# Performance work log

Hardware: AMD Instinct MI355X
Metric: run time of the kernel (lower is better)

## Reference

```python
import jax, jax.numpy as jnp
import numpy as np

D_IN = 256
DIMS = 256


def setup_inputs() -> dict:
    key = jax.random.key(0)
    k1, k2, k3, k4, k5 = jax.random.split(key, 5)
    B, Tq, Tk = 4, 512, 512
    query = jax.random.normal(k1, (B, Tq, D_IN), dtype=jnp.float32)
    value = jax.random.normal(k2, (B, Tk, D_IN), dtype=jnp.float32)
    # Dense(dims, use_bias=False) kernels (glorot-like scale) and AdditiveAttention scale vector
    Wq = jax.random.normal(k3, (D_IN, DIMS), dtype=jnp.float32) / np.sqrt(D_IN)
    Wv = jax.random.normal(k4, (D_IN, DIMS), dtype=jnp.float32) / np.sqrt(D_IN)
    scale = jax.random.normal(k5, (DIMS,), dtype=jnp.float32)
    return {"query": query, "value": value, "Wq": Wq, "Wv": Wv, "scale": scale}


def reference(query, value, Wq, Wv, scale):
    # q_proj: [B,Tq,d], k_proj: [B,Tk,d]; attention value = RAW value tensor (as in source)
    q = jnp.einsum("bqi,id->bqd", query, Wq)
    k = jnp.einsum("bki,id->bkd", value, Wv)
    # Additive (Bahdanau) scores: [B,Tq,Tk] via broadcast tanh then reduce with scale
    scores = jnp.einsum("bqkd,d->bqk", jnp.tanh(q[:, :, None, :] + k[:, None, :, :]), scale)
    attn = jax.nn.softmax(scores, axis=-1)  # masks are all-ones -> no-op
    out = jnp.einsum("bqk,bki->bqi", attn, value)
    return out, attn
```

## Files before the change

### kernel.cpp

```cpp
#include <hip/hip_runtime.h>

#define LOG2E 1.4426950408889634f
#define TWO_LOG2E 2.885390081777927f

__device__ __forceinline__ float fast_exp2(float x) { return __builtin_amdgcn_exp2f(x); }
__device__ __forceinline__ float fast_rcp(float x)  { return __builtin_amdgcn_rcpf(x); }

__global__ __launch_bounds__(256) void proj_kernel(
    const float* __restrict__ query, const float* __restrict__ value,
    const float* __restrict__ Wq, const float* __restrict__ Wv,
    float* __restrict__ eq, float* __restrict__ ek)
{
    __shared__ float in_lds[8 * 256];
    const int t = threadIdx.x;
    const int row0 = blockIdx.x * 8;
    const float* src; const float* W; float* dst;
    if (row0 < 2048) { src = query + (size_t)row0 * 256; W = Wq; dst = eq + (size_t)row0 * 256; }
    else { const int r = row0 - 2048; src = value + (size_t)r * 256; W = Wv; dst = ek + (size_t)r * 256; }

    const float4* s4 = (const float4*)src;
    float4* l4 = (float4*)in_lds;
    l4[t] = s4[t];
    l4[t + 256] = s4[t + 256];
    __syncthreads();

    float acc[8];
#pragma unroll
    for (int r = 0; r < 8; ++r) acc[r] = 0.f;

    for (int d = 0; d < 256; d += 4) {
        const float w0 = W[(d + 0) * 256 + t];
        const float w1 = W[(d + 1) * 256 + t];
        const float w2 = W[(d + 2) * 256 + t];
        const float w3 = W[(d + 3) * 256 + t];
#pragma unroll
        for (int r = 0; r < 8; ++r) {
            const float4 v = *(const float4*)&in_lds[r * 256 + d];
            acc[r] = fmaf(v.x, w0, acc[r]);
            acc[r] = fmaf(v.y, w1, acc[r]);
            acc[r] = fmaf(v.z, w2, acc[r]);
            acc[r] = fmaf(v.w, w3, acc[r]);
        }
    }
#pragma unroll
    for (int r = 0; r < 8; ++r) dst[r * 256 + t] = fast_exp2(acc[r] * TWO_LOG2E);
}

#define SQ_ST 130
__global__ __launch_bounds__(512) void scores_kernel(
    const float* __restrict__ eq, const float* __restrict__ ek,
    const float* __restrict__ scale, float* __restrict__ sraw)
{
    __shared__ float q_lds[32 * SQ_ST];
    __shared__ float k_lds[64 * SQ_ST];
    __shared__ float sc_lds[256];

    const int t = threadIdx.x;
    const int tx = t & 31, ty = t >> 5;
    const int ktg = blockIdx.x, qt = blockIdx.y, b = blockIdx.z;
    const float* qbase = eq + (size_t)(b * 512 + qt * 32) * 256;
    const float* kbase = ek + (size_t)(b * 512 + ktg * 64) * 256;

    if (t < 256) sc_lds[t] = -2.f * scale[t];

    float a00 = 0.f, a01 = 0.f, a10 = 0.f, a11 = 0.f;

    for (int dc = 0; dc < 256; dc += 128) {
        __syncthreads();
#pragma unroll
        for (int l = 0; l < 2; ++l) {
            const int idx = t + 512 * l;
            const int row = idx >> 5, c4 = (idx & 31) * 4;
            const float4 v = *(const float4*)&qbase[row * 256 + dc + c4];
            *(float2*)&q_lds[row * SQ_ST + c4]     = make_float2(v.x, v.y);
            *(float2*)&q_lds[row * SQ_ST + c4 + 2] = make_float2(v.z, v.w);
        }
#pragma unroll
        for (int l = 0; l < 4; ++l) {
            const int idx = t + 512 * l;
            const int row = idx >> 5, c4 = (idx & 31) * 4;
            const float4 v = *(const float4*)&kbase[row * 256 + dc + c4];
            *(float2*)&k_lds[row * SQ_ST + c4]     = make_float2(v.x, v.y);
            *(float2*)&k_lds[row * SQ_ST + c4 + 2] = make_float2(v.z, v.w);
        }
        __syncthreads();

#pragma unroll 4
        for (int d = 0; d < 128; d += 2) {
            const float2 s2 = *(const float2*)&sc_lds[dc + d];
            const float2 qa = *(const float2*)&q_lds[(ty * 2 + 0) * SQ_ST + d];
            const float2 qb = *(const float2*)&q_lds[(ty * 2 + 1) * SQ_ST + d];
            const float2 ka = *(const float2*)&k_lds[tx * SQ_ST + d];
            const float2 kb = *(const float2*)&k_lds[(tx + 32) * SQ_ST + d];

            {
                const float A = fmaf(qa.x, ka.x, 1.f), B = fmaf(qa.y, ka.y, 1.f);
                a00 = fmaf(fmaf(s2.y, A, s2.x * B), fast_rcp(A * B), a00);
            }
            {
                const float A = fmaf(qa.x, kb.x, 1.f), B = fmaf(qa.y, kb.y, 1.f);
                a01 = fmaf(fmaf(s2.y, A, s2.x * B), fast_rcp(A * B), a01);
            }
            {
                const float A = fmaf(qb.x, ka.x, 1.f), B = fmaf(qb.y, ka.y, 1.f);
                a10 = fmaf(fmaf(s2.y, A, s2.x * B), fast_rcp(A * B), a10);
            }
            {
                const float A = fmaf(qb.x, kb.x, 1.f), B = fmaf(qb.y, kb.y, 1.f);
                a11 = fmaf(fmaf(s2.y, A, s2.x * B), fast_rcp(A * B), a11);
            }
        }
    }

    const int qrow = b * 512 + qt * 32 + ty * 2;
    const int kcol = ktg * 64 + tx;
    sraw[(size_t)(qrow + 0) * 512 + kcol]      = a00;
    sraw[(size_t)(qrow + 0) * 512 + kcol + 32] = a01;
    sraw[(size_t)(qrow + 1) * 512 + kcol]      = a10;
    sraw[(size_t)(qrow + 1) * 512 + kcol + 32] = a11;
}

#define SS_ROW 516
__global__ __launch_bounds__(512) void softpv_kernel(
    float* __restrict__ attn, const float* __restrict__ value,
    float* __restrict__ out)
{
    __shared__ float s_lds[8 * SS_ROW];
    __shared__ float red[4 * 8 * 256];
    __shared__ float inv_lds[8];

    const int t = threadIdx.x;
    const int w = t >> 6, lane = t & 63;
    const int qt = blockIdx.x, b = blockIdx.y;
    const int q0 = qt * 8;
    float* srow = attn + (size_t)(b * 512 + q0 + w) * 512;

    float e[8];
    float m = -1e30f;
#pragma unroll
    for (int j = 0; j < 8; ++j) {
        e[j] = srow[lane + 64 * j];
        m = fmaxf(m, e[j]);
    }
#pragma unroll
    for (int off = 32; off; off >>= 1) m = fmaxf(m, __shfl_xor(m, off));

    float sum = 0.f;
#pragma unroll
    for (int j = 0; j < 8; ++j) {
        e[j] = fast_exp2((e[j] - m) * LOG2E);
        sum += e[j];
    }
#pragma unroll
    for (int off = 32; off; off >>= 1) sum += __shfl_xor(sum, off);

    const float inv = fast_rcp(sum);
#pragma unroll
    for (int j = 0; j < 8; ++j) {
        s_lds[w * SS_ROW + lane + 64 * j] = e[j];
        srow[lane + 64 * j] = e[j] * inv;
    }
    if (lane == 0) inv_lds[w] = inv;
    __syncthreads();

    float4 acc[8];
#pragma unroll
    for (int r = 0; r < 8; ++r) acc[r] = make_float4(0.f, 0.f, 0.f, 0.f);

    const float* vbase = value + (size_t)(b * 512 + 64 * w) * 256;
    for (int k4 = 0; k4 < 64; k4 += 4) {
        const float4 v0 = *(const float4*)&vbase[(k4 + 0) * 256 + lane * 4];
        const float4 v1 = *(const float4*)&vbase[(k4 + 1) * 256 + lane * 4];
        const float4 v2 = *(const float4*)&vbase[(k4 + 2) * 256 + lane * 4];
        const float4 v3 = *(const float4*)&vbase[(k4 + 3) * 256 + lane * 4];
#pragma unroll
        for (int r = 0; r < 8; ++r) {
            const float4 s4 = *(const float4*)&s_lds[r * SS_ROW + 64 * w + k4];
            acc[r].x = fmaf(s4.x, v0.x, acc[r].x); acc[r].y = fmaf(s4.x, v0.y, acc[r].y);
            acc[r].z = fmaf(s4.x, v0.z, acc[r].z); acc[r].w = fmaf(s4.x, v0.w, acc[r].w);
            acc[r].x = fmaf(s4.y, v1.x, acc[r].x); acc[r].y = fmaf(s4.y, v1.y, acc[r].y);
            acc[r].z = fmaf(s4.y, v1.z, acc[r].z); acc[r].w = fmaf(s4.y, v1.w, acc[r].w);
            acc[r].x = fmaf(s4.z, v2.x, acc[r].x); acc[r].y = fmaf(s4.z, v2.y, acc[r].y);
            acc[r].z = fmaf(s4.z, v2.z, acc[r].z); acc[r].w = fmaf(s4.z, v2.w, acc[r].w);
            acc[r].x = fmaf(s4.w, v3.x, acc[r].x); acc[r].y = fmaf(s4.w, v3.y, acc[r].y);
            acc[r].z = fmaf(s4.w, v3.z, acc[r].z); acc[r].w = fmaf(s4.w, v3.w, acc[r].w);
        }
    }

    if (w >= 4) {
#pragma unroll
        for (int r = 0; r < 8; ++r)
            *(float4*)&red[((w - 4) * 8 + r) * 256 + lane * 4] = acc[r];
    }
    __syncthreads();
    if (w < 4) {
#pragma unroll
        for (int r = 0; r < 8; ++r) {
            const float4 o = *(const float4*)&red[(w * 8 + r) * 256 + lane * 4];
            acc[r].x += o.x; acc[r].y += o.y; acc[r].z += o.z; acc[r].w += o.w;
        }
    }
    __syncthreads();
    if (w >= 2 && w < 4) {
#pragma unroll
        for (int r = 0; r < 8; ++r)
            *(float4*)&red[((w - 2) * 8 + r) * 256 + lane * 4] = acc[r];
    }
    __syncthreads();
    if (w < 2) {
#pragma unroll
        for (int r = 0; r < 8; ++r) {
            const float4 o = *(const float4*)&red[(w * 8 + r) * 256 + lane * 4];
            acc[r].x += o.x; acc[r].y += o.y; acc[r].z += o.z; acc[r].w += o.w;
        }
    }
    __syncthreads();
    if (w == 1) {
#pragma unroll
        for (int r = 0; r < 8; ++r)
            *(float4*)&red[r * 256 + lane * 4] = acc[r];
    }
    __syncthreads();
    if (w == 0) {
#pragma unroll
        for (int r = 0; r < 8; ++r) {
            const float4 o = *(const float4*)&red[r * 256 + lane * 4];
            const float iv = inv_lds[r];
            float4 res;
            res.x = (acc[r].x + o.x) * iv;
            res.y = (acc[r].y + o.y) * iv;
            res.z = (acc[r].z + o.z) * iv;
            res.w = (acc[r].w + o.w) * iv;
            *(float4*)&out[(size_t)(b * 512 + q0 + r) * 256 + lane * 4] = res;
        }
    }
}

extern "C" void kernel_launch(void* const* d_in, const int* in_sizes, int n_in,
                              void* d_out, int out_size, void* d_ws, size_t ws_size,
                              hipStream_t stream) {
    const float* query = (const float*)d_in[0];
    const float* value = (const float*)d_in[1];
    const float* Wq    = (const float*)d_in[2];
    const float* Wv    = (const float*)d_in[3];
    const float* scale = (const float*)d_in[4];

    float* out0 = (float*)d_out;
    float* attn = out0 + 4 * 512 * 256;

    float* eq = (float*)d_ws;
    float* ek = eq + 2048 * 256;

    proj_kernel<<<512, 256, 0, stream>>>(query, value, Wq, Wv, eq, ek);
    scores_kernel<<<dim3(8, 16, 4), 512, 0, stream>>>(eq, ek, scale, attn);
    softpv_kernel<<<dim3(64, 4), 512, 0, stream>>>(attn, value, out0);
}
```

Baseline: 69.76 us.

## Fuse additive-score computation with softmax and PV into one kernel

Merges the separate scores kernel into the softmax/PV kernel. Each block now computes the full score rows for its 8 queries by streaming all 512 keys of its batch through LDS in 64-row tiles, then runs softmax and the PV product. This removes the raw-score round trip through global memory and one kernel launch. In exchange, each block reloads the batch's entire key projection from L2, gets less register reuse per score (one output per thread instead of four), and runs the scores phase on only 256 blocks with no overlap between loads and compute.

```diff
diff --git a/kernel.cpp b/kernel.cpp
--- a/kernel.cpp
+++ b/kernel.cpp
@@ -46,119 +46,83 @@
     for (int r = 0; r < 8; ++r) dst[r * 256 + t] = fast_exp2(acc[r] * TWO_LOG2E);
 }
 
-#define SQ_ST 130
-__global__ __launch_bounds__(512) void scores_kernel(
+#define EK_ST 258
+#define EQ_ST 258
+#define SS_ROW 516
+__global__ __launch_bounds__(512) void fused_kernel(
     const float* __restrict__ eq, const float* __restrict__ ek,
-    const float* __restrict__ scale, float* __restrict__ sraw)
+    const float* __restrict__ scale, const float* __restrict__ value,
+    float* __restrict__ attn, float* __restrict__ out)
 {
-    __shared__ float q_lds[32 * SQ_ST];
-    __shared__ float k_lds[64 * SQ_ST];
+    __shared__ float ek_lds[64 * EK_ST];
+    __shared__ float eq_lds[8 * EQ_ST];
     __shared__ float sc_lds[256];
-
-    const int t = threadIdx.x;
-    const int tx = t & 31, ty = t >> 5;
-    const int ktg = blockIdx.x, qt = blockIdx.y, b = blockIdx.z;
-    const float* qbase = eq + (size_t)(b * 512 + qt * 32) * 256;
-    const float* kbase = ek + (size_t)(b * 512 + ktg * 64) * 256;
-
-    if (t < 256) sc_lds[t] = -2.f * scale[t];
-
-    float a00 = 0.f, a01 = 0.f, a10 = 0.f, a11 = 0.f;
-
-    for (int dc = 0; dc < 256; dc += 128) {
-        __syncthreads();
-#pragma unroll
-        for (int l = 0; l < 2; ++l) {
-            const int idx = t + 512 * l;
-            const int row = idx >> 5, c4 = (idx & 31) * 4;
-            const float4 v = *(const float4*)&qbase[row * 256 + dc + c4];
-            *(float2*)&q_lds[row * SQ_ST + c4]     = make_float2(v.x, v.y);
-            *(float2*)&q_lds[row * SQ_ST + c4 + 2] = make_float2(v.z, v.w);
-        }
-#pragma unroll
-        for (int l = 0; l < 4; ++l) {
-            const int idx = t + 512 * l;
-            const int row = idx >> 5, c4 = (idx & 31) * 4;
-            const float4 v = *(const float4*)&kbase[row * 256 + dc + c4];
-            *(float2*)&k_lds[row * SQ_ST + c4]     = make_float2(v.x, v.y);
-            *(float2*)&k_lds[row * SQ_ST + c4 + 2] = make_float2(v.z, v.w);
-        }
-        __syncthreads();
-
-#pragma unroll 4
-        for (int d = 0; d < 128; d += 2) {
-            const float2 s2 = *(const float2*)&sc_lds[dc + d];
-            const float2 qa = *(const float2*)&q_lds[(ty * 2 + 0) * SQ_ST + d];
-            const float2 qb = *(const float2*)&q_lds[(ty * 2 + 1) * SQ_ST + d];
-            const float2 ka = *(const float2*)&k_lds[tx * SQ_ST + d];
-            const float2 kb = *(const float2*)&k_lds[(tx + 32) * SQ_ST + d];
-
-            {
-                const float A = fmaf(qa.x, ka.x, 1.f), B = fmaf(qa.y, ka.y, 1.f);
-                a00 = fmaf(fmaf(s2.y, A, s2.x * B), fast_rcp(A * B), a00);
-            }
-            {
-                const float A = fmaf(qa.x, kb.x, 1.f), B = fmaf(qa.y, kb.y, 1.f);
-                a01 = fmaf(fmaf(s2.y, A, s2.x * B), fast_rcp(A * B), a01);
-            }
-            {
-                const float A = fmaf(qb.x, ka.x, 1.f), B = fmaf(qb.y, ka.y, 1.f);
-                a10 = fmaf(fmaf(s2.y, A, s2.x * B), fast_rcp(A * B), a10);
-            }
-            {
-                const float A = fmaf(qb.x, kb.x, 1.f), B = fmaf(qb.y, kb.y, 1.f);
-                a11 = fmaf(fmaf(s2.y, A, s2.x * B), fast_rcp(A * B), a11);
-            }
-        }
-    }
-
-    const int qrow = b * 512 + qt * 32 + ty * 2;
-    const int kcol = ktg * 64 + tx;
-    sraw[(size_t)(qrow + 0) * 512 + kcol]      = a00;
-    sraw[(size_t)(qrow + 0) * 512 + kcol + 32] = a01;
-    sraw[(size_t)(qrow + 1) * 512 + kcol]      = a10;
-    sraw[(size_t)(qrow + 1) * 512 + kcol + 32] = a11;
-}
-
-#define SS_ROW 516
-__global__ __launch_bounds__(512) void softpv_kernel(
-    float* __restrict__ attn, const float* __restrict__ value,
-    float* __restrict__ out)
-{
     __shared__ float s_lds[8 * SS_ROW];
-    __shared__ float red[4 * 8 * 256];
     __shared__ float inv_lds[8];
 
     const int t = threadIdx.x;
     const int w = t >> 6, lane = t & 63;
     const int qt = blockIdx.x, b = blockIdx.y;
     const int q0 = qt * 8;
-    float* srow = attn + (size_t)(b * 512 + q0 + w) * 512;
+
+    {
+        const float4 v = *((const float4*)(eq + (size_t)(b * 512 + q0) * 256) + t);
+        const int row = t >> 6, c4 = (t & 63) * 4;
+        *(float2*)&eq_lds[row * EQ_ST + c4]     = make_float2(v.x, v.y);
+        *(float2*)&eq_lds[row * EQ_ST + c4 + 2] = make_float2(v.z, v.w);
+    }
+    if (t < 256) sc_lds[t] = -2.f * scale[t];
 
     float e[8];
+    const float* ekb = ek + (size_t)(b * 512) * 256;
+
+#pragma unroll
+    for (int tt = 0; tt < 8; ++tt) {
+        __syncthreads();
+        const float4* src = (const float4*)(ekb + (size_t)(64 * tt) * 256);
+#pragma unroll
+        for (int l = 0; l < 8; ++l) {
+            const int idx = t + 512 * l;
+            const int row = idx >> 6, c4 = (idx & 63) * 4;
+            const float4 v = src[idx];
+            *(float2*)&ek_lds[row * EK_ST + c4]     = make_float2(v.x, v.y);
+            *(float2*)&ek_lds[row * EK_ST + c4 + 2] = make_float2(v.z, v.w);
+        }
+        __syncthreads();
+
+        float acc = 0.f;
+        const float* eqrow = &eq_lds[w * EQ_ST];
+        const float* ekrow = &ek_lds[lane * EK_ST];
+#pragma unroll 4
+        for (int d = 0; d < 256; d += 2) {
+            const float2 s2 = *(const float2*)&sc_lds[d];
+            const float2 qv = *(const float2*)&eqrow[d];
+            const float2 kv = *(const float2*)&ekrow[d];
+            const float A = fmaf(qv.x, kv.x, 1.f);
+            const float B = fmaf(qv.y, kv.y, 1.f);
+            acc = fmaf(fmaf(s2.y, A, s2.x * B), fast_rcp(A * B), acc);
+        }
+        e[tt] = acc;
+    }
+
     float m = -1e30f;
 #pragma unroll
+    for (int j = 0; j < 8; ++j) m = fmaxf(m, e[j]);
+#pragma unroll
+    for (int off = 32; off; off >>= 1) m = fmaxf(m, __shfl_xor(m, off));
+
+    float sum = 0.f;
+#pragma unroll
+    for (int j = 0; j < 8; ++j) { e[j] = fast_exp2((e[j] - m) * LOG2E); sum += e[j]; }
+#pragma unroll
+    for (int off = 32; off; off >>= 1) sum += __shfl_xor(sum, off);
+    const float inv = fast_rcp(sum);
+
+    float* arow = attn + (size_t)(b * 512 + q0 + w) * 512;
+#pragma unroll
     for (int j = 0; j < 8; ++j) {
-        e[j] = srow[lane + 64 * j];
-        m = fmaxf(m, e[j]);
-    }
-#pragma unroll
-    for (int off = 32; off; off >>= 1) m = fmaxf(m, __shfl_xor(m, off));
-
-    float sum = 0.f;
-#pragma unroll
-    for (int j = 0; j < 8; ++j) {
-        e[j] = fast_exp2((e[j] - m) * LOG2E);
-        sum += e[j];
-    }
-#pragma unroll
-    for (int off = 32; off; off >>= 1) sum += __shfl_xor(sum, off);
-
-    const float inv = fast_rcp(sum);
-#pragma unroll
-    for (int j = 0; j < 8; ++j) {
-        s_lds[w * SS_ROW + lane + 64 * j] = e[j];
-        srow[lane + 64 * j] = e[j] * inv;
+        s_lds[w * SS_ROW + 64 * j + lane] = e[j];
+        arow[64 * j + lane] = e[j] * inv;
     }
     if (lane == 0) inv_lds[w] = inv;
     __syncthreads();
@@ -187,6 +151,7 @@
         }
     }
 
+    float* red = ek_lds;
     if (w >= 4) {
 #pragma unroll
         for (int r = 0; r < 8; ++r)
@@ -252,6 +217,5 @@
     float* ek = eq + 2048 * 256;
 
     proj_kernel<<<512, 256, 0, stream>>>(query, value, Wq, Wv, eq, ek);
-    scores_kernel<<<dim3(8, 16, 4), 512, 0, stream>>>(eq, ek, scale, attn);
-    softpv_kernel<<<dim3(64, 4), 512, 0, stream>>>(attn, value, out0);
+    fused_kernel<<<dim3(64, 4), 512, 0, stream>>>(eq, ek, scale, value, attn, out0);
 }
```

Result: slower. 80.48 us (+15.4%).
